# Optimization experiments

Measured on AMD Instinct MI355X. Metric: run time of the kernel, lower is better.

Reference implementation:

```python
import jax, jax.numpy as jnp
import numpy as np

N_NODES = 100000
N_EDGES = 1600000
IN_DIM = 64
F1, F2, F3 = 64, 64, 32
EPS = 1e-12  # torch F.normalize eps


def _glorot(key, shape):
    fan_in, fan_out = shape[0], shape[1]
    lim = (6.0 / (fan_in + fan_out)) ** 0.5
    return jax.random.uniform(key, shape, jnp.float32, -lim, lim)


def setup_inputs() -> dict:
    key = jax.random.key(0)
    ks = jax.random.split(key, 16)
    features_1 = jax.random.normal(ks[0], (N_NODES, IN_DIM), jnp.float32)
    edge_index_1 = jax.random.randint(ks[1], (2, N_EDGES), 0, N_NODES, jnp.int64)
    return {
        "features_1": features_1,
        "edge_index_1": edge_index_1,
        # SAGEConv 1: lin_l (aggregated, with bias), lin_r (root, no bias)
        "W1l": _glorot(ks[2], (IN_DIM, F1)), "b1": jnp.zeros((F1,), jnp.float32), "W1r": _glorot(ks[3], (IN_DIM, F1)),
        "W2l": _glorot(ks[4], (F1, F2)), "b2": jnp.zeros((F2,), jnp.float32), "W2r": _glorot(ks[5], (F1, F2)),
        "W3l": _glorot(ks[6], (F2, F3)), "b3": jnp.zeros((F3,), jnp.float32), "W3r": _glorot(ks[7], (F2, F3)),
        # SimGNN attention pooling weight [F3, F3]
        "W_att": _glorot(ks[8], (F3, F3)),
        # MLP head
        "W_fc": _glorot(ks[9], (F3, 16)), "b_fc": jnp.zeros((16,), jnp.float32),
        "W_s": _glorot(ks[10], (16, 1)), "b_s": jnp.zeros((1,), jnp.float32),
    }


def _sage_conv(x, src, tgt, Wl, b, Wr):
    # mean-aggregate source features at target nodes (PyG SAGEConv, aggr='mean')
    msg_sum = jax.ops.segment_sum(x[src], tgt, num_segments=N_NODES)  # [N, F]
    deg = jax.ops.segment_sum(jnp.ones((src.shape[0],), x.dtype), tgt, num_segments=N_NODES)
    agg = msg_sum / jnp.maximum(deg, 1.0)[:, None]
    out = agg @ Wl + b + x @ Wr
    # normalize=True -> L2 normalize per node
    norm = jnp.linalg.norm(out, axis=-1, keepdims=True)
    return out / jnp.maximum(norm, EPS)


def reference(features_1, edge_index_1, W1l, b1, W1r, W2l, b2, W2r, W3l, b3, W3r, W_att, W_fc, b_fc, W_s, b_s):
    src, tgt = edge_index_1[0], edge_index_1[1]
    h = _sage_conv(features_1, src, tgt, W1l, b1, W1r)
    h = jax.nn.relu(h)  # dropout p=0 / eval mode -> identity
    h = _sage_conv(h, src, tgt, W2l, b2, W2r)
    h = jax.nn.relu(h)
    h = _sage_conv(h, src, tgt, W3l, b3, W3r)  # [N, F3]
    # SimGNN attention pooling
    context = jnp.tanh(jnp.mean(h @ W_att, axis=0))          # [F3]
    att = jax.nn.sigmoid(h @ context)                         # [N]
    pooled = (att @ h)[None, :]                               # [1, F3]
    hidden = jax.nn.relu(pooled @ W_fc + b_fc)                # [1, 16]
    score = jax.nn.sigmoid(hidden @ W_s + b_s)                # [1, 1]
    return score
```

## Files before the change

kernel.cpp:

```cpp
#include <hip/hip_runtime.h>
#include <hip/hip_bf16.h>
#include <hip/hip_fp16.h>
#include <math.h>

#define N_NODES 100000
#define N_EDGES 1600000
#define SCAN_BLOCKS 98
#define XCD_RANGE 12500

typedef _Float16 h8 __attribute__((ext_vector_type(8)));
typedef float f32x4 __attribute__((ext_vector_type(4)));

__device__ __forceinline__ float bcast(float v, int l) {
    return __int_as_float(__builtin_amdgcn_readlane(__float_as_int(v), l));
}

__global__ __launch_bounds__(256) void k_cvt(const float* __restrict__ in,
                                             _Float16* __restrict__ out) {
    int i = blockIdx.x * 256 + threadIdx.x;
    const f32x4* p = reinterpret_cast<const f32x4*>(in) + (size_t)i * 2;
    f32x4 u = __builtin_nontemporal_load(p);
    f32x4 v = __builtin_nontemporal_load(p + 1);
    h8 o;
    o[0] = u[0]; o[1] = u[1]; o[2] = u[2]; o[3] = u[3];
    o[4] = v[0]; o[5] = v[1]; o[6] = v[2]; o[7] = v[3];
    *(reinterpret_cast<h8*>(out) + i) = o;
}

__global__ __launch_bounds__(256) void k_count(const int* __restrict__ tgt,
                                               int* __restrict__ counts) {
    int p = blockIdx.x & 7;
    int e = (blockIdx.x >> 3) * 256 + threadIdx.x;
    int t = __builtin_nontemporal_load(tgt + e);
    if ((unsigned)(t - p * XCD_RANGE) < XCD_RANGE) atomicAdd(&counts[t], 1);
}

__global__ __launch_bounds__(256) void k_scanA(const int* __restrict__ counts,
                                               int* __restrict__ rowptr,
                                               int* __restrict__ bsum) {
    int t = threadIdx.x;
    int base = blockIdx.x * 1024 + t * 4;
    int v0 = (base + 0 < N_NODES) ? counts[base + 0] : 0;
    int v1 = (base + 1 < N_NODES) ? counts[base + 1] : 0;
    int v2 = (base + 2 < N_NODES) ? counts[base + 2] : 0;
    int v3 = (base + 3 < N_NODES) ? counts[base + 3] : 0;
    int s = v0 + v1 + v2 + v3;
    __shared__ int sS[256];
    sS[t] = s;
    __syncthreads();
    for (int off = 1; off < 256; off <<= 1) {
        int add = (t >= off) ? sS[t - off] : 0;
        __syncthreads();
        sS[t] += add;
        __syncthreads();
    }
    int excl = sS[t] - s;
    if (t == 255) bsum[blockIdx.x] = sS[255];
    if (base + 0 < N_NODES) rowptr[base + 0] = excl;
    if (base + 1 < N_NODES) rowptr[base + 1] = excl + v0;
    if (base + 2 < N_NODES) rowptr[base + 2] = excl + v0 + v1;
    if (base + 3 < N_NODES) rowptr[base + 3] = excl + v0 + v1 + v2;
}

__global__ void k_scanB(const int* __restrict__ bsum, int* __restrict__ boff) {
    __shared__ int sD[128];
    int t = threadIdx.x;
    int v = (t < SCAN_BLOCKS) ? bsum[t] : 0;
    sD[t] = v;
    __syncthreads();
    for (int off = 1; off < 128; off <<= 1) {
        int add = (t >= off) ? sD[t - off] : 0;
        __syncthreads();
        sD[t] += add;
        __syncthreads();
    }
    boff[t] = sD[t] - v;
}

__global__ __launch_bounds__(256) void k_scanC(int* __restrict__ rowptr,
                                               const int* __restrict__ boff) {
    int t = threadIdx.x;
    int base = blockIdx.x * 1024 + t * 4;
    int add = boff[blockIdx.x];
    if (base + 0 < N_NODES) rowptr[base + 0] += add;
    if (base + 1 < N_NODES) rowptr[base + 1] += add;
    if (base + 2 < N_NODES) rowptr[base + 2] += add;
    if (base + 3 < N_NODES) rowptr[base + 3] += add;
}

__global__ __launch_bounds__(256) void k_fill(const int* __restrict__ ei,
                                              int* __restrict__ rowptr,
                                              int* __restrict__ csr) {
    int p = blockIdx.x & 7;
    int e = (blockIdx.x >> 3) * 256 + threadIdx.x;
    int t = __builtin_nontemporal_load(ei + N_EDGES + e);
    if ((unsigned)(t - p * XCD_RANGE) < XCD_RANGE) {
        int s = __builtin_nontemporal_load(ei + e);
        int pos = atomicAdd(&rowptr[t], 1);
        csr[pos] = s;
    }
}

template <int LD>
__device__ __forceinline__ void gadd(float (&A)[8], const _Float16* __restrict__ x,
                                     int idx, int n, int cnt, int c8) {
    int s = __shfl(idx, n);
    h8 v = *reinterpret_cast<const h8*>(x + (size_t)s * LD + c8);
    float m = (n < cnt) ? 1.0f : 0.0f;
#pragma unroll
    for (int j = 0; j < 8; ++j) A[j] = fmaf((float)v[j], m, A[j]);
}

__global__ __launch_bounds__(256) void k_gather64(const _Float16* __restrict__ x,
                                                  const int* __restrict__ rowptr,
                                                  const int* __restrict__ csr,
                                                  _Float16* __restrict__ agg) {
    int wid = (blockIdx.x * 256 + threadIdx.x) >> 6;
    int lane = threadIdx.x & 63;
    if (wid >= N_NODES) return;
    int rs = (wid > 0) ? rowptr[wid - 1] : 0;
    int re = rowptr[wid];
    int sub = lane >> 3;
    int c8 = (lane & 7) * 8;
    float a0[8] = {0}, a1[8] = {0}, a2[8] = {0}, a3[8] = {0};
    for (int base = rs; base < re; base += 64) {
        int j = base + lane;
        int idx = (j < re) ? csr[j] : 0;
        int cnt = min(64, re - base);
        {
            gadd<64>(a0, x, idx, 0 + sub, cnt, c8);
            gadd<64>(a1, x, idx, 8 + sub, cnt, c8);
        }
        if (16 < cnt) {
            gadd<64>(a2, x, idx, 16 + sub, cnt, c8);
            gadd<64>(a3, x, idx, 24 + sub, cnt, c8);
        }
        if (32 < cnt) {
            gadd<64>(a0, x, idx, 32 + sub, cnt, c8);
            gadd<64>(a1, x, idx, 40 + sub, cnt, c8);
        }
        if (48 < cnt) {
            gadd<64>(a2, x, idx, 48 + sub, cnt, c8);
            gadd<64>(a3, x, idx, 56 + sub, cnt, c8);
        }
    }
    float acc[8];
#pragma unroll
    for (int j = 0; j < 8; ++j) acc[j] = (a0[j] + a1[j]) + (a2[j] + a3[j]);
#pragma unroll
    for (int m = 8; m <= 32; m <<= 1) {
#pragma unroll
        for (int j = 0; j < 8; ++j) acc[j] += __shfl_xor(acc[j], m);
    }
    if (lane < 8) {
        float invd = 1.0f / fmaxf((float)(re - rs), 1.0f);
        h8 o;
#pragma unroll
        for (int j = 0; j < 8; ++j) o[j] = (_Float16)(acc[j] * invd);
        *reinterpret_cast<h8*>(agg + (size_t)wid * 64 + c8) = o;
    }
}

__global__ __launch_bounds__(256) void k_gather32(const _Float16* __restrict__ z,
                                                  const int* __restrict__ rowptr,
                                                  const int* __restrict__ csr,
                                                  _Float16* __restrict__ agg) {
    int wid = (blockIdx.x * 256 + threadIdx.x) >> 6;
    int lane = threadIdx.x & 63;
    if (wid >= N_NODES) return;
    int rs = (wid > 0) ? rowptr[wid - 1] : 0;
    int re = rowptr[wid];
    int sub = lane >> 2;
    int c8 = (lane & 3) * 8;
    float a0[8] = {0}, a1[8] = {0}, a2[8] = {0}, a3[8] = {0};
    for (int base = rs; base < re; base += 64) {
        int j = base + lane;
        int idx = (j < re) ? csr[j] : 0;
        int cnt = min(64, re - base);
        gadd<32>(a0, z, idx, 0 + sub, cnt, c8);
        if (16 < cnt) gadd<32>(a1, z, idx, 16 + sub, cnt, c8);
        if (32 < cnt) gadd<32>(a2, z, idx, 32 + sub, cnt, c8);
        if (48 < cnt) gadd<32>(a3, z, idx, 48 + sub, cnt, c8);
    }
    float acc[8];
#pragma unroll
    for (int j = 0; j < 8; ++j) acc[j] = (a0[j] + a1[j]) + (a2[j] + a3[j]);
#pragma unroll
    for (int m = 4; m <= 32; m <<= 1) {
#pragma unroll
        for (int j = 0; j < 8; ++j) acc[j] += __shfl_xor(acc[j], m);
    }
    if (lane < 4) {
        float invd = 1.0f / fmaxf((float)(re - rs), 1.0f);
        h8 o;
#pragma unroll
        for (int j = 0; j < 8; ++j) o[j] = (_Float16)(acc[j] * invd);
        *reinterpret_cast<h8*>(agg + (size_t)wid * 32 + c8) = o;
    }
}

template <bool RELU>
__global__ __launch_bounds__(256) void k_xform64m(const _Float16* __restrict__ x,
                                                  const _Float16* __restrict__ agg,
                                                  const float* __restrict__ Wl,
                                                  const float* __restrict__ b,
                                                  const float* __restrict__ Wr,
                                                  _Float16* __restrict__ out) {
    int lane = threadIdx.x & 63;
    int g = lane >> 4;
    int r = lane & 15;
    int wv = (blockIdx.x * 256 + threadIdx.x) >> 6;
    int nw = gridDim.x * 4;
    h8 wl[2][4], wr[2][4];
#pragma unroll
    for (int kt = 0; kt < 2; ++kt)
#pragma unroll
        for (int ct = 0; ct < 4; ++ct)
#pragma unroll
            for (int j = 0; j < 8; ++j) {
                int row = kt * 32 + g * 8 + j, col = ct * 16 + r;
                wl[kt][ct][j] = (_Float16)Wl[row * 64 + col];
                wr[kt][ct][j] = (_Float16)Wr[row * 64 + col];
            }
    float biasv[4];
#pragma unroll
    for (int ct = 0; ct < 4; ++ct) biasv[ct] = b[ct * 16 + r];
    for (int tile = wv; tile < N_NODES / 16; tile += nw) {
        int n0 = tile * 16;
        const h8* arow = reinterpret_cast<const h8*>(agg + (size_t)(n0 + r) * 64);
        const h8* xrow = reinterpret_cast<const h8*>(x + (size_t)(n0 + r) * 64);
        h8 aa0 = arow[g], aa1 = arow[4 + g];
        h8 ax0 = xrow[g], ax1 = xrow[4 + g];
        f32x4 acc[4];
#pragma unroll
        for (int ct = 0; ct < 4; ++ct) {
            acc[ct] = (f32x4){biasv[ct], biasv[ct], biasv[ct], biasv[ct]};
            acc[ct] = __builtin_amdgcn_mfma_f32_16x16x32_f16(aa0, wl[0][ct], acc[ct], 0, 0, 0);
            acc[ct] = __builtin_amdgcn_mfma_f32_16x16x32_f16(aa1, wl[1][ct], acc[ct], 0, 0, 0);
            acc[ct] = __builtin_amdgcn_mfma_f32_16x16x32_f16(ax0, wr[0][ct], acc[ct], 0, 0, 0);
            acc[ct] = __builtin_amdgcn_mfma_f32_16x16x32_f16(ax1, wr[1][ct], acc[ct], 0, 0, 0);
        }
#pragma unroll
        for (int reg = 0; reg < 4; ++reg) {
            float ss = acc[0][reg] * acc[0][reg] + acc[1][reg] * acc[1][reg] +
                       acc[2][reg] * acc[2][reg] + acc[3][reg] * acc[3][reg];
            ss += __shfl_xor(ss, 1);
            ss += __shfl_xor(ss, 2);
            ss += __shfl_xor(ss, 4);
            ss += __shfl_xor(ss, 8);
            float rinv = 1.0f / fmaxf(sqrtf(ss), 1e-12f);
            int row = n0 + g * 4 + reg;
#pragma unroll
            for (int ct = 0; ct < 4; ++ct) {
                float v = acc[ct][reg] * rinv;
                if (RELU) v = fmaxf(v, 0.0f);
                out[(size_t)row * 64 + ct * 16 + r] = (_Float16)v;
            }
        }
    }
}

__global__ __launch_bounds__(256, 2) void k_pretrans(const _Float16* __restrict__ x,
                                                     const float* __restrict__ W,
                                                     _Float16* __restrict__ z) {
    int lane = threadIdx.x & 63;
    int o = lane & 31;
    int h = lane >> 5;
    int wv = (blockIdx.x * 256 + threadIdx.x) >> 6;
    int nw = gridDim.x * 4;
    float wc[32];
#pragma unroll
    for (int j = 0; j < 32; ++j) wc[j] = W[(h * 32 + j) * 32 + o];
    for (int node = wv; node < N_NODES; node += nw) {
        float xr = (float)x[(size_t)node * 64 + lane];
        float acc = 0.f;
#pragma unroll
        for (int j = 0; j < 32; ++j) {
            float blo = bcast(xr, j);
            float bhi = bcast(xr, j + 32);
            acc = fmaf(h ? bhi : blo, wc[j], acc);
        }
        acc += __shfl_xor(acc, 32);
        if (lane < 32) z[(size_t)node * 32 + o] = (_Float16)acc;
    }
}

__global__ __launch_bounds__(256, 2) void k_fin3(const _Float16* __restrict__ x,
                                                 const _Float16* __restrict__ agg32,
                                                 const float* __restrict__ b,
                                                 const float* __restrict__ Wr,
                                                 float* __restrict__ out,
                                                 float* __restrict__ colsum) {
    int lane = threadIdx.x & 63;
    int o = lane & 31;
    int h = lane >> 5;
    int wave = threadIdx.x >> 6;
    int wv = (blockIdx.x * 256 + threadIdx.x) >> 6;
    int nw = gridDim.x * 4;
    float wc[32];
#pragma unroll
    for (int j = 0; j < 32; ++j) wc[j] = Wr[(h * 32 + j) * 32 + o];
    float breg = b[o];
    float csacc = 0.f;
    for (int node = wv; node < N_NODES; node += nw) {
        float xr = (float)x[(size_t)node * 64 + lane];
        float acc = 0.f;
#pragma unroll
        for (int j = 0; j < 32; ++j) {
            float blo = bcast(xr, j);
            float bhi = bcast(xr, j + 32);
            acc = fmaf(h ? bhi : blo, wc[j], acc);
        }
        acc += __shfl_xor(acc, 32);
        float val = acc + (float)agg32[(size_t)node * 32 + o] + breg;
        float ss = val * val;
#pragma unroll
        for (int m = 16; m; m >>= 1) ss += __shfl_xor(ss, m);
        float ov = val / fmaxf(sqrtf(ss), 1e-12f);
        if (lane < 32) {
            out[(size_t)node * 32 + o] = ov;
            csacc += ov;
        }
    }
    __shared__ float sCS[4][32];
    if (lane < 32) sCS[wave][o] = csacc;
    __syncthreads();
    if (threadIdx.x < 32) {
        float v = sCS[0][threadIdx.x] + sCS[1][threadIdx.x] +
                  sCS[2][threadIdx.x] + sCS[3][threadIdx.x];
        atomicAdd(&colsum[threadIdx.x], v);
    }
}

__global__ __launch_bounds__(256) void k_attpool(const float* __restrict__ h,
                                                 const float* __restrict__ colsum,
                                                 const float* __restrict__ Watt,
                                                 float* __restrict__ pooled) {
    __shared__ float sC[32];
    __shared__ float sP[4][32];
    int t = threadIdx.x;
    if (t < 32) {
        float acc = 0.0f;
#pragma unroll
        for (int f = 0; f < 32; ++f)
            acc += (colsum[f] * (1.0f / N_NODES)) * Watt[f * 32 + t];
        sC[t] = tanhf(acc);
    }
    __syncthreads();
    float p[32];
#pragma unroll
    for (int f = 0; f < 32; ++f) p[f] = 0.f;
    int stride = gridDim.x * 256;
    for (int n = blockIdx.x * 256 + t; n < N_NODES; n += stride) {
        const f32x4* row = reinterpret_cast<const f32x4*>(h + (size_t)n * 32);
        f32x4 r[8];
        float dot = 0.0f;
#pragma unroll
        for (int q = 0; q < 8; ++q) {
            r[q] = row[q];
            dot += r[q][0] * sC[q * 4] + r[q][1] * sC[q * 4 + 1] +
                   r[q][2] * sC[q * 4 + 2] + r[q][3] * sC[q * 4 + 3];
        }
        float att = 1.0f / (1.0f + expf(-dot));
#pragma unroll
        for (int q = 0; q < 8; ++q) {
            p[q * 4 + 0] = fmaf(att, r[q][0], p[q * 4 + 0]);
            p[q * 4 + 1] = fmaf(att, r[q][1], p[q * 4 + 1]);
            p[q * 4 + 2] = fmaf(att, r[q][2], p[q * 4 + 2]);
            p[q * 4 + 3] = fmaf(att, r[q][3], p[q * 4 + 3]);
        }
    }
#pragma unroll
    for (int f = 0; f < 32; ++f) {
#pragma unroll
        for (int m = 1; m < 64; m <<= 1) p[f] += __shfl_xor(p[f], m);
    }
    int wave = t >> 6, lane = t & 63;
    if (lane == 0) {
#pragma unroll
        for (int f = 0; f < 32; ++f) sP[wave][f] = p[f];
    }
    __syncthreads();
    if (t < 32) {
        float v = sP[0][t] + sP[1][t] + sP[2][t] + sP[3][t];
        atomicAdd(&pooled[t], v);
    }
}

__global__ void k_head(const float* __restrict__ pooled,
                       const float* __restrict__ Wfc, const float* __restrict__ bfc,
                       const float* __restrict__ Ws, const float* __restrict__ bs,
                       float* __restrict__ out) {
    __shared__ float sH[16];
    int t = threadIdx.x;
    if (t < 16) {
        float acc = bfc[t];
#pragma unroll
        for (int f = 0; f < 32; ++f) acc += pooled[f] * Wfc[f * 16 + t];
        sH[t] = fmaxf(acc, 0.0f);
    }
    __syncthreads();
    if (t == 0) {
        float s = bs[0];
#pragma unroll
        for (int j = 0; j < 16; ++j) s += sH[j] * Ws[j];
        out[0] = 1.0f / (1.0f + expf(-s));
    }
}

extern "C" void kernel_launch(void* const* d_in, const int* in_sizes, int n_in,
                              void* d_out, int out_size, void* d_ws, size_t ws_size,
                              hipStream_t stream) {
    const float* feat = (const float*)d_in[0];
    const int* ei = (const int*)d_in[1];
    const float* W1l = (const float*)d_in[2];
    const float* b1 = (const float*)d_in[3];
    const float* W1r = (const float*)d_in[4];
    const float* W2l = (const float*)d_in[5];
    const float* b2 = (const float*)d_in[6];
    const float* W2r = (const float*)d_in[7];
    const float* W3l = (const float*)d_in[8];
    const float* b3 = (const float*)d_in[9];
    const float* W3r = (const float*)d_in[10];
    const float* Watt = (const float*)d_in[11];
    const float* Wfc = (const float*)d_in[12];
    const float* bfc = (const float*)d_in[13];
    const float* Ws = (const float*)d_in[14];
    const float* bs = (const float*)d_in[15];
    float* out = (float*)d_out;

    int* rowptr = (int*)d_ws;
    int* bsum = rowptr + 100000;
    int* boff = bsum + 128;
    int* counts = boff + 128;
    int* csr = counts + 100000;
    _Float16* B1 = (_Float16*)(csr + N_EDGES);
    _Float16* B2 = B1 + (size_t)N_NODES * 64;
    _Float16* B3 = B2 + (size_t)N_NODES * 64;
    float* h3 = (float*)(B3 + (size_t)N_NODES * 64);
    float* colsum = h3 + (size_t)N_NODES * 32;
    float* pooled = colsum + 32;

    hipMemsetAsync(counts, 0, N_NODES * sizeof(int), stream);
    hipMemsetAsync(colsum, 0, 64 * sizeof(float), stream);
    k_cvt<<<3125, 256, 0, stream>>>(feat, B1);
    k_count<<<(N_EDGES / 256) * 8, 256, 0, stream>>>(ei + N_EDGES, counts);
    k_scanA<<<SCAN_BLOCKS, 256, 0, stream>>>(counts, rowptr, bsum);
    k_scanB<<<1, 128, 0, stream>>>(bsum, boff);
    k_scanC<<<SCAN_BLOCKS, 256, 0, stream>>>(rowptr, boff);
    k_fill<<<(N_EDGES / 256) * 8, 256, 0, stream>>>(ei, rowptr, csr);

    k_gather64<<<25000, 256, 0, stream>>>(B1, rowptr, csr, B2);
    k_xform64m<true><<<512, 256, 0, stream>>>(B1, B2, W1l, b1, W1r, B3);

    k_gather64<<<25000, 256, 0, stream>>>(B3, rowptr, csr, B2);
    k_xform64m<true><<<512, 256, 0, stream>>>(B3, B2, W2l, b2, W2r, B1);

    _Float16* z = B3;
    _Float16* agg32 = B3 + (size_t)N_NODES * 32;
    k_pretrans<<<1024, 256, 0, stream>>>(B1, W3l, z);
    k_gather32<<<25000, 256, 0, stream>>>(z, rowptr, csr, agg32);
    k_fin3<<<1024, 256, 0, stream>>>(B1, agg32, b3, W3r, h3, colsum);

    k_attpool<<<391, 256, 0, stream>>>(h3, colsum, Watt, pooled);
    k_head<<<1, 64, 0, stream>>>(pooled, Wfc, bfc, Ws, bs, out);
}
```

Baseline: 524.0 us.

## Fuse layer-3 projections into layer-2 MFMA transform and gather with finalize

The layer-2 MFMA transform now also computes the layer-3 projections h@W3l and h@W3r with MFMA, staging the normalized ReLU tile through shared memory. This replaces the scalar readlane-based pretrans and fin3 kernels. The 32-wide gather now finishes layer 3 directly by adding the root term and bias, L2-normalizing, and writing h3. That removes an intermediate HBM round trip and a launch. Column sums move to a separate reduction kernel that re-reads h3, which adds a pass over 12.8 MB.

```diff
diff --git a/kernel.cpp b/kernel.cpp
--- a/kernel.cpp
+++ b/kernel.cpp
@@ -161,44 +161,6 @@
     }
 }
 
-__global__ __launch_bounds__(256) void k_gather32(const _Float16* __restrict__ z,
-                                                  const int* __restrict__ rowptr,
-                                                  const int* __restrict__ csr,
-                                                  _Float16* __restrict__ agg) {
-    int wid = (blockIdx.x * 256 + threadIdx.x) >> 6;
-    int lane = threadIdx.x & 63;
-    if (wid >= N_NODES) return;
-    int rs = (wid > 0) ? rowptr[wid - 1] : 0;
-    int re = rowptr[wid];
-    int sub = lane >> 2;
-    int c8 = (lane & 3) * 8;
-    float a0[8] = {0}, a1[8] = {0}, a2[8] = {0}, a3[8] = {0};
-    for (int base = rs; base < re; base += 64) {
-        int j = base + lane;
-        int idx = (j < re) ? csr[j] : 0;
-        int cnt = min(64, re - base);
-        gadd<32>(a0, z, idx, 0 + sub, cnt, c8);
-        if (16 < cnt) gadd<32>(a1, z, idx, 16 + sub, cnt, c8);
-        if (32 < cnt) gadd<32>(a2, z, idx, 32 + sub, cnt, c8);
-        if (48 < cnt) gadd<32>(a3, z, idx, 48 + sub, cnt, c8);
-    }
-    float acc[8];
-#pragma unroll
-    for (int j = 0; j < 8; ++j) acc[j] = (a0[j] + a1[j]) + (a2[j] + a3[j]);
-#pragma unroll
-    for (int m = 4; m <= 32; m <<= 1) {
-#pragma unroll
-        for (int j = 0; j < 8; ++j) acc[j] += __shfl_xor(acc[j], m);
-    }
-    if (lane < 4) {
-        float invd = 1.0f / fmaxf((float)(re - rs), 1.0f);
-        h8 o;
-#pragma unroll
-        for (int j = 0; j < 8; ++j) o[j] = (_Float16)(acc[j] * invd);
-        *reinterpret_cast<h8*>(agg + (size_t)wid * 32 + c8) = o;
-    }
-}
-
 template <bool RELU>
 __global__ __launch_bounds__(256) void k_xform64m(const _Float16* __restrict__ x,
                                                   const _Float16* __restrict__ agg,
@@ -260,74 +222,173 @@
     }
 }
 
-__global__ __launch_bounds__(256, 2) void k_pretrans(const _Float16* __restrict__ x,
-                                                     const float* __restrict__ W,
-                                                     _Float16* __restrict__ z) {
+__global__ __launch_bounds__(256) void k_xform64z(const _Float16* __restrict__ x,
+                                                  const _Float16* __restrict__ agg,
+                                                  const float* __restrict__ Wl,
+                                                  const float* __restrict__ b,
+                                                  const float* __restrict__ Wr,
+                                                  const float* __restrict__ W3l,
+                                                  const float* __restrict__ W3r,
+                                                  _Float16* __restrict__ z,
+                                                  _Float16* __restrict__ r3) {
     int lane = threadIdx.x & 63;
-    int o = lane & 31;
-    int h = lane >> 5;
+    int g = lane >> 4;
+    int r = lane & 15;
+    int wv4 = threadIdx.x >> 6;
     int wv = (blockIdx.x * 256 + threadIdx.x) >> 6;
     int nw = gridDim.x * 4;
-    float wc[32];
-#pragma unroll
-    for (int j = 0; j < 32; ++j) wc[j] = W[(h * 32 + j) * 32 + o];
-    for (int node = wv; node < N_NODES; node += nw) {
-        float xr = (float)x[(size_t)node * 64 + lane];
-        float acc = 0.f;
-#pragma unroll
-        for (int j = 0; j < 32; ++j) {
-            float blo = bcast(xr, j);
-            float bhi = bcast(xr, j + 32);
-            acc = fmaf(h ? bhi : blo, wc[j], acc);
-        }
-        acc += __shfl_xor(acc, 32);
-        if (lane < 32) z[(size_t)node * 32 + o] = (_Float16)acc;
-    }
-}
-
-__global__ __launch_bounds__(256, 2) void k_fin3(const _Float16* __restrict__ x,
-                                                 const _Float16* __restrict__ agg32,
-                                                 const float* __restrict__ b,
-                                                 const float* __restrict__ Wr,
-                                                 float* __restrict__ out,
-                                                 float* __restrict__ colsum) {
+    __shared__ _Float16 sT[4][16][72];
+    h8 wl[2][4], wr[2][4];
+#pragma unroll
+    for (int kt = 0; kt < 2; ++kt)
+#pragma unroll
+        for (int ct = 0; ct < 4; ++ct)
+#pragma unroll
+            for (int j = 0; j < 8; ++j) {
+                int row = kt * 32 + g * 8 + j, col = ct * 16 + r;
+                wl[kt][ct][j] = (_Float16)Wl[row * 64 + col];
+                wr[kt][ct][j] = (_Float16)Wr[row * 64 + col];
+            }
+    h8 wz[2][2], w3[2][2];
+#pragma unroll
+    for (int kt = 0; kt < 2; ++kt)
+#pragma unroll
+        for (int ct = 0; ct < 2; ++ct)
+#pragma unroll
+            for (int j = 0; j < 8; ++j) {
+                int row = kt * 32 + g * 8 + j, col = ct * 16 + r;
+                wz[kt][ct][j] = (_Float16)W3l[row * 32 + col];
+                w3[kt][ct][j] = (_Float16)W3r[row * 32 + col];
+            }
+    float biasv[4];
+#pragma unroll
+    for (int ct = 0; ct < 4; ++ct) biasv[ct] = b[ct * 16 + r];
+    for (int tile = wv; tile < N_NODES / 16; tile += nw) {
+        int n0 = tile * 16;
+        const h8* arow = reinterpret_cast<const h8*>(agg + (size_t)(n0 + r) * 64);
+        const h8* xrow = reinterpret_cast<const h8*>(x + (size_t)(n0 + r) * 64);
+        h8 aa0 = arow[g], aa1 = arow[4 + g];
+        h8 ax0 = xrow[g], ax1 = xrow[4 + g];
+        f32x4 acc[4];
+#pragma unroll
+        for (int ct = 0; ct < 4; ++ct) {
+            acc[ct] = (f32x4){biasv[ct], biasv[ct], biasv[ct], biasv[ct]};
+            acc[ct] = __builtin_amdgcn_mfma_f32_16x16x32_f16(aa0, wl[0][ct], acc[ct], 0, 0, 0);
+            acc[ct] = __builtin_amdgcn_mfma_f32_16x16x32_f16(aa1, wl[1][ct], acc[ct], 0, 0, 0);
+            acc[ct] = __builtin_amdgcn_mfma_f32_16x16x32_f16(ax0, wr[0][ct], acc[ct], 0, 0, 0);
+            acc[ct] = __builtin_amdgcn_mfma_f32_16x16x32_f16(ax1, wr[1][ct], acc[ct], 0, 0, 0);
+        }
+#pragma unroll
+        for (int reg = 0; reg < 4; ++reg) {
+            float ss = acc[0][reg] * acc[0][reg] + acc[1][reg] * acc[1][reg] +
+                       acc[2][reg] * acc[2][reg] + acc[3][reg] * acc[3][reg];
+            ss += __shfl_xor(ss, 1);
+            ss += __shfl_xor(ss, 2);
+            ss += __shfl_xor(ss, 4);
+            ss += __shfl_xor(ss, 8);
+            float rinv = 1.0f / fmaxf(sqrtf(ss), 1e-12f);
+            int row16 = g * 4 + reg;
+#pragma unroll
+            for (int ct = 0; ct < 4; ++ct) {
+                float v = fmaxf(acc[ct][reg] * rinv, 0.0f);
+                sT[wv4][row16][ct * 16 + r] = (_Float16)v;
+            }
+        }
+        h8 ha0 = *reinterpret_cast<const h8*>(&sT[wv4][r][g * 8]);
+        h8 ha1 = *reinterpret_cast<const h8*>(&sT[wv4][r][32 + g * 8]);
+        f32x4 zacc[2], racc[2];
+#pragma unroll
+        for (int ct = 0; ct < 2; ++ct) {
+            zacc[ct] = (f32x4){0, 0, 0, 0};
+            zacc[ct] = __builtin_amdgcn_mfma_f32_16x16x32_f16(ha0, wz[0][ct], zacc[ct], 0, 0, 0);
+            zacc[ct] = __builtin_amdgcn_mfma_f32_16x16x32_f16(ha1, wz[1][ct], zacc[ct], 0, 0, 0);
+            racc[ct] = (f32x4){0, 0, 0, 0};
+            racc[ct] = __builtin_amdgcn_mfma_f32_16x16x32_f16(ha0, w3[0][ct], racc[ct], 0, 0, 0);
+            racc[ct] = __builtin_amdgcn_mfma_f32_16x16x32_f16(ha1, w3[1][ct], racc[ct], 0, 0, 0);
+        }
+#pragma unroll
+        for (int reg = 0; reg < 4; ++reg) {
+            int row = n0 + g * 4 + reg;
+#pragma unroll
+            for (int ct = 0; ct < 2; ++ct) {
+                z[(size_t)row * 32 + ct * 16 + r] = (_Float16)zacc[ct][reg];
+                r3[(size_t)row * 32 + ct * 16 + r] = (_Float16)racc[ct][reg];
+            }
+        }
+    }
+}
+
+__global__ __launch_bounds__(256) void k_g32fin(const _Float16* __restrict__ z,
+                                                const int* __restrict__ rowptr,
+                                                const int* __restrict__ csr,
+                                                const _Float16* __restrict__ r3,
+                                                const float* __restrict__ b3,
+                                                float* __restrict__ h3) {
+    int wid = (blockIdx.x * 256 + threadIdx.x) >> 6;
     int lane = threadIdx.x & 63;
-    int o = lane & 31;
-    int h = lane >> 5;
-    int wave = threadIdx.x >> 6;
-    int wv = (blockIdx.x * 256 + threadIdx.x) >> 6;
-    int nw = gridDim.x * 4;
-    float wc[32];
-#pragma unroll
-    for (int j = 0; j < 32; ++j) wc[j] = Wr[(h * 32 + j) * 32 + o];
-    float breg = b[o];
-    float csacc = 0.f;
-    for (int node = wv; node < N_NODES; node += nw) {
-        float xr = (float)x[(size_t)node * 64 + lane];
-        float acc = 0.f;
-#pragma unroll
-        for (int j = 0; j < 32; ++j) {
-            float blo = bcast(xr, j);
-            float bhi = bcast(xr, j + 32);
-            acc = fmaf(h ? bhi : blo, wc[j], acc);
-        }
-        acc += __shfl_xor(acc, 32);
-        float val = acc + (float)agg32[(size_t)node * 32 + o] + breg;
-        float ss = val * val;
-#pragma unroll
-        for (int m = 16; m; m >>= 1) ss += __shfl_xor(ss, m);
-        float ov = val / fmaxf(sqrtf(ss), 1e-12f);
-        if (lane < 32) {
-            out[(size_t)node * 32 + o] = ov;
-            csacc += ov;
-        }
-    }
-    __shared__ float sCS[4][32];
-    if (lane < 32) sCS[wave][o] = csacc;
+    if (wid >= N_NODES) return;
+    int sub = lane >> 2;
+    int c8 = (lane & 3) * 8;
+    float bb[8];
+#pragma unroll
+    for (int j = 0; j < 8; ++j) bb[j] = b3[c8 + j];
+    int rs = (wid > 0) ? rowptr[wid - 1] : 0;
+    int re = rowptr[wid];
+    float a0[8] = {0}, a1[8] = {0}, a2[8] = {0}, a3[8] = {0};
+    for (int base = rs; base < re; base += 64) {
+        int j = base + lane;
+        int idx = (j < re) ? csr[j] : 0;
+        int cnt = min(64, re - base);
+        gadd<32>(a0, z, idx, 0 + sub, cnt, c8);
+        if (16 < cnt) gadd<32>(a1, z, idx, 16 + sub, cnt, c8);
+        if (32 < cnt) gadd<32>(a2, z, idx, 32 + sub, cnt, c8);
+        if (48 < cnt) gadd<32>(a3, z, idx, 48 + sub, cnt, c8);
+    }
+    float acc[8];
+#pragma unroll
+    for (int j = 0; j < 8; ++j) acc[j] = (a0[j] + a1[j]) + (a2[j] + a3[j]);
+#pragma unroll
+    for (int m = 4; m <= 32; m <<= 1) {
+#pragma unroll
+        for (int j = 0; j < 8; ++j) acc[j] += __shfl_xor(acc[j], m);
+    }
+    float invd = 1.0f / fmaxf((float)(re - rs), 1.0f);
+    h8 rr = (lane < 4) ? *reinterpret_cast<const h8*>(r3 + (size_t)wid * 32 + c8)
+                       : (h8){0, 0, 0, 0, 0, 0, 0, 0};
+    float val[8];
+    float ss = 0.f;
+#pragma unroll
+    for (int j = 0; j < 8; ++j) {
+        val[j] = fmaf(acc[j], invd, (float)rr[j] + bb[j]);
+        ss = fmaf(val[j], val[j], ss);
+    }
+    ss += __shfl_xor(ss, 1);
+    ss += __shfl_xor(ss, 2);
+    if (lane < 4) {
+        float rinv = 1.0f / fmaxf(sqrtf(ss), 1e-12f);
+        f32x4 o0 = {val[0] * rinv, val[1] * rinv, val[2] * rinv, val[3] * rinv};
+        f32x4 o1 = {val[4] * rinv, val[5] * rinv, val[6] * rinv, val[7] * rinv};
+        f32x4* op = reinterpret_cast<f32x4*>(h3 + (size_t)wid * 32 + c8);
+        op[0] = o0;
+        op[1] = o1;
+    }
+}
+
+__global__ __launch_bounds__(256) void k_colsum(const float* __restrict__ h,
+                                                float* __restrict__ colsum) {
+    int gid = blockIdx.x * 256 + threadIdx.x;
+    const int total = N_NODES * 32;
+    const int stride = 1024 * 256;
+    float s = 0.0f;
+    for (int i = gid; i < total; i += stride) s += h[i];
+    s += __shfl_xor(s, 32);
+    __shared__ float sP[4][32];
+    int wave = threadIdx.x >> 6, lane = threadIdx.x & 63;
+    if (lane < 32) sP[wave][lane] = s;
     __syncthreads();
     if (threadIdx.x < 32) {
-        float v = sCS[0][threadIdx.x] + sCS[1][threadIdx.x] +
-                  sCS[2][threadIdx.x] + sCS[3][threadIdx.x];
+        float v = sP[0][threadIdx.x] + sP[1][threadIdx.x] + sP[2][threadIdx.x] +
+                  sP[3][threadIdx.x];
         atomicAdd(&colsum[threadIdx.x], v);
     }
 }
@@ -453,15 +514,14 @@
     k_gather64<<<25000, 256, 0, stream>>>(B1, rowptr, csr, B2);
     k_xform64m<true><<<512, 256, 0, stream>>>(B1, B2, W1l, b1, W1r, B3);
 
+    _Float16* z = B1;
+    _Float16* r3 = B1 + (size_t)N_NODES * 32;
     k_gather64<<<25000, 256, 0, stream>>>(B3, rowptr, csr, B2);
-    k_xform64m<true><<<512, 256, 0, stream>>>(B3, B2, W2l, b2, W2r, B1);
-
-    _Float16* z = B3;
-    _Float16* agg32 = B3 + (size_t)N_NODES * 32;
-    k_pretrans<<<1024, 256, 0, stream>>>(B1, W3l, z);
-    k_gather32<<<25000, 256, 0, stream>>>(z, rowptr, csr, agg32);
-    k_fin3<<<1024, 256, 0, stream>>>(B1, agg32, b3, W3r, h3, colsum);
-
+    k_xform64z<<<512, 256, 0, stream>>>(B3, B2, W2l, b2, W2r, W3l, W3r, z, r3);
+
+    k_g32fin<<<25000, 256, 0, stream>>>(z, rowptr, csr, r3, b3, h3);
+
+    k_colsum<<<1024, 256, 0, stream>>>(h3, colsum);
     k_attpool<<<391, 256, 0, stream>>>(h3, colsum, Watt, pooled);
     k_head<<<1, 64, 0, stream>>>(pooled, Wfc, bfc, Ws, bs, out);
 }
```

New measurement: 464.0 us. 1.13x faster.
